# Kernel optimization log

Hardware: AMD Instinct MI355X
Metric: run time of the kernel (lower is better)

## Reference

```python
import jax, jax.numpy as jnp
import numpy as np

NUM_HEADS = 16

def _apply_rope(x, cos, sin):
    # x: (B, H, T, D); cos/sin: (T, D//2)
    B, H, T, D = x.shape
    xr = x.reshape(B, H, T, D // 2, 2)
    x0, x1 = xr[..., 0], xr[..., 1]
    c = cos[None, None, :, :]
    s = sin[None, None, :, :]
    out = jnp.stack([x0 * c - x1 * s, x0 * s + x1 * c], axis=-1)
    return out.reshape(B, H, T, D)


def setup_inputs() -> dict:
    key = jax.random.key(0)
    k1, k2, k3 = jax.random.split(key, 3)
    B, T, C = 2, 2048, 1024
    D = C // NUM_HEADS
    x = jax.random.normal(k1, (B, T, C), dtype=jnp.float32)
    qkv_w = jax.random.normal(k2, (3 * C, C), dtype=jnp.float32) * (C ** -0.5)
    proj_w = jax.random.normal(k3, (C, C), dtype=jnp.float32) * (C ** -0.5)
    # standard RoPE frequency table (theta = 10000)
    inv_freq = 1.0 / (10000.0 ** (jnp.arange(0, D, 2, dtype=jnp.float32) / D))  # (D/2,)
    angles = jnp.arange(T, dtype=jnp.float32)[:, None] * inv_freq[None, :]      # (T, D/2)
    return {
        "x": x,
        "freqs_cos": jnp.cos(angles),
        "freqs_sin": jnp.sin(angles),
        "qkv_w": qkv_w,
        "proj_w": proj_w,
    }


def reference(x, freqs_cos, freqs_sin, qkv_w, proj_w):
    B, T, C = x.shape
    H = NUM_HEADS
    D = C // H
    qkv = x @ qkv_w.T                                  # (B, T, 3C)
    q, k, v = jnp.split(qkv, 3, axis=-1)
    q = q.reshape(B, T, H, D).transpose(0, 2, 1, 3)    # (B, H, T, D)
    k = k.reshape(B, T, H, D).transpose(0, 2, 1, 3)
    v = v.reshape(B, T, H, D).transpose(0, 2, 1, 3)
    q = _apply_rope(q, freqs_cos, freqs_sin)
    k = _apply_rope(k, freqs_cos, freqs_sin)
    scale = 1.0 / jnp.sqrt(jnp.asarray(D, dtype=x.dtype))
    scores = jnp.einsum('bhqd,bhkd->bhqk', q, k) * scale
    causal = jnp.tril(jnp.ones((T, T), dtype=bool))
    scores = jnp.where(causal[None, None], scores, jnp.finfo(scores.dtype).min)
    attn = jax.nn.softmax(scores, axis=-1)
    out = jnp.einsum('bhqk,bhkd->bhqd', attn, v)       # (B, H, T, D)
    out = out.transpose(0, 2, 1, 3).reshape(B, T, C)
    return out @ proj_w.T
```

## Files before the change

kernel.cpp:

```cpp
#include <hip/hip_runtime.h>
#include <stdint.h>

#define DI __device__ __forceinline__

typedef unsigned short u16;
typedef __bf16 bf16x8 __attribute__((ext_vector_type(8)));
typedef unsigned short u16x8 __attribute__((ext_vector_type(8)));
typedef unsigned short u16x4 __attribute__((ext_vector_type(4)));
typedef float f32x4 __attribute__((ext_vector_type(4)));

DI u16 f2bf(float f) { __bf16 h = (__bf16)f; return __builtin_bit_cast(u16, h); }
DI float bf2f(u16 u) { return (float)__builtin_bit_cast(__bf16, u); }

DI bf16x8 ld8(const u16* p) { return __builtin_bit_cast(bf16x8, *(const u16x8*)p); }

DI f32x4 mfma16(bf16x8 a, bf16x8 b, f32x4 c) {
  return __builtin_amdgcn_mfma_f32_16x16x32_bf16(a, b, c, 0, 0, 0);
}

DI void async16(const u16* g, u16* l) {
  __builtin_amdgcn_global_load_lds((const __attribute__((address_space(1))) void*)g,
                                   (__attribute__((address_space(3))) void*)l, 16, 0, 0);
}

__global__ __launch_bounds__(256) void cast_all(const float* __restrict__ x,
                                                const float* __restrict__ qw,
                                                const float* __restrict__ pw,
                                                u16* __restrict__ xb, u16* __restrict__ qwb,
                                                u16* __restrict__ pwb) {
  const int bi = blockIdx.x;
  const float* src;
  u16* dst;
  int off;
  if (bi < 4096) {
    src = x; dst = xb; off = bi;
  } else if (bi < 7168) {
    src = qw; dst = qwb; off = bi - 4096;
  } else {
    src = pw; dst = pwb; off = bi - 7168;
  }
  const int i = off * 256 + threadIdx.x;
  const float4 v = ((const float4*)src)[i];
  u16x4 o = {f2bf(v.x), f2bf(v.y), f2bf(v.z), f2bf(v.w)};
  ((u16x4*)dst)[i] = o;
}

template <int OUT_BF16>
__global__ __launch_bounds__(256) void gemm_bt(const u16* __restrict__ A,
                                               const u16* __restrict__ W,
                                               void* __restrict__ outp,
                                               int M, int N, int K) {
  __shared__ u16 sA[2 * 4096];
  __shared__ u16 sB[2 * 4096];
  const int tid = threadIdx.x;
  const int w = tid >> 6, L = tid & 63;
  const int lo = L & 15, quad = L >> 4;
  const int nb = N >> 7;
  const int bm = blockIdx.x / nb, bn = blockIdx.x - bm * nb;
  const int m0 = bm << 7, n0 = bn << 7;
  const int wm = (w >> 1) << 6, wn = (w & 1) << 6;

  f32x4 acc[4][4];
#pragma unroll
  for (int i = 0; i < 4; ++i)
#pragma unroll
    for (int j = 0; j < 4; ++j) acc[i][j] = 0.f;

  const int r0 = tid >> 2, s0 = tid & 3;
  const int c0 = s0 ^ ((r0 >> 1) & 3);
  const int r1 = r0 + 64;
  const int c1 = s0 ^ ((r1 >> 1) & 3);
  const u16* aP0 = A + (size_t)(m0 + r0) * K + c0 * 8;
  const u16* aP1 = A + (size_t)(m0 + r1) * K + c1 * 8;
  const u16* bP0 = W + (size_t)(n0 + r0) * K + c0 * 8;
  const u16* bP1 = W + (size_t)(n0 + r1) * K + c1 * 8;
  u16* ldA0 = &sA[tid * 8];
  u16* ldA1 = &sA[(tid + 256) * 8];
  u16* ldB0 = &sB[tid * 8];
  u16* ldB1 = &sB[(tid + 256) * 8];

  int raf[4], rbf[4];
#pragma unroll
  for (int mt = 0; mt < 4; ++mt) {
    int r = wm + mt * 16 + lo;
    raf[mt] = r * 32 + ((quad ^ ((r >> 1) & 3)) << 3);
    r = wn + mt * 16 + lo;
    rbf[mt] = r * 32 + ((quad ^ ((r >> 1) & 3)) << 3);
  }

  auto stage = [&](int buf) {
    const int bo = buf << 12;
    async16(aP0, ldA0 + bo);
    async16(aP1, ldA1 + bo);
    async16(bP0, ldB0 + bo);
    async16(bP1, ldB1 + bo);
    aP0 += 32; aP1 += 32; bP0 += 32; bP1 += 32;
  };

  const int kIters = K >> 5;
  stage(0);
  for (int kt = 0; kt < kIters; ++kt) {
    __syncthreads();
    if (kt + 1 < kIters) stage((kt + 1) & 1);
    const int bo = (kt & 1) << 12;
    bf16x8 af[4], bfr[4];
#pragma unroll
    for (int mt = 0; mt < 4; ++mt) af[mt] = ld8(&sA[bo + raf[mt]]);
#pragma unroll
    for (int nt = 0; nt < 4; ++nt) bfr[nt] = ld8(&sB[bo + rbf[nt]]);
#pragma unroll
    for (int mt = 0; mt < 4; ++mt)
#pragma unroll
      for (int nt = 0; nt < 4; ++nt)
        acc[mt][nt] = mfma16(af[mt], bfr[nt], acc[mt][nt]);
  }

#pragma unroll
  for (int mt = 0; mt < 4; ++mt) {
    const int m = m0 + wm + mt * 16 + quad * 4;
#pragma unroll
    for (int nt = 0; nt < 4; ++nt) {
      const int n = n0 + wn + nt * 16 + lo;
#pragma unroll
      for (int r = 0; r < 4; ++r) {
        const size_t off = (size_t)(m + r) * N + n;
        if (OUT_BF16)
          ((u16*)outp)[off] = f2bf(acc[mt][nt][r]);
        else
          ((float*)outp)[off] = acc[mt][nt][r];
      }
    }
  }
}

#define QSCALE 0.18033688011112f
__global__ __launch_bounds__(256) void ropevt_k(const u16* __restrict__ qkv,
                                                const float* __restrict__ cosb,
                                                const float* __restrict__ sinb,
                                                u16* __restrict__ qo, u16* __restrict__ ko,
                                                u16* __restrict__ vto) {
  __shared__ u16 sT[64 * 64];
  const int tid = threadIdx.x;
  if (blockIdx.x < 8192) {
    const int idx = blockIdx.x * 256 + tid;
    const int i = idx & 31;
    const int t = (idx >> 5) & 2047;
    const int h = (idx >> 16) & 15;
    const int b = idx >> 20;
    const size_t src = ((size_t)(b * 2048 + t)) * 3072 + h * 64 + 2 * i;
    const float q0v = bf2f(qkv[src]), q1v = bf2f(qkv[src + 1]);
    const float k0v = bf2f(qkv[src + 1024]), k1v = bf2f(qkv[src + 1025]);
    const float c = cosb[t * 32 + i], s = sinb[t * 32 + i];
    const size_t dst = ((size_t)((b * 16 + h) * 2048 + t)) * 64 + 2 * i;
    qo[dst] = f2bf((q0v * c - q1v * s) * QSCALE);
    qo[dst + 1] = f2bf((q0v * s + q1v * c) * QSCALE);
    ko[dst] = f2bf(k0v * c - k1v * s);
    ko[dst + 1] = f2bf(k0v * s + k1v * c);
  } else {
    const int bi = blockIdx.x - 8192;
    const int bh = bi & 31;
    const int t0 = (bi >> 5) << 6;
    const int b = bh >> 4, h = bh & 15;
#pragma unroll
    for (int it = 0; it < 2; ++it) {
      const int id = tid + it * 256;
      const int tr = id >> 3, s = id & 7, c = s ^ (tr & 7);
      async16(qkv + (size_t)(b * 2048 + t0 + tr) * 3072 + 2048 + h * 64 + c * 8, &sT[id * 8]);
    }
    __syncthreads();
#pragma unroll
    for (int it = 0; it < 2; ++it) {
      const int id = tid + it * 256;
      const int d = id >> 3, ct = id & 7;
      u16x8 o;
#pragma unroll
      for (int j = 0; j < 8; ++j) {
        const int t = ct * 8 + j;
        o[j] = sT[t * 64 + (((d >> 3) ^ (t & 7)) << 3) + (d & 7)];
      }
      *(u16x8*)(vto + ((size_t)bh * 64 + d) * 2048 + t0 + ct * 8) = o;
    }
  }
}

__global__ __launch_bounds__(256) void fattn_part(const u16* __restrict__ qs,
                                                  const u16* __restrict__ ks,
                                                  const u16* __restrict__ vtb,
                                                  u16* __restrict__ opart,
                                                  float* __restrict__ lbuf) {
  __shared__ u16 sK[2 * 4096];
  __shared__ u16 sVt[2 * 4096];
  __shared__ u16 sP[4][16 * 64];
  const int tid = threadIdx.x;
  const int w = tid >> 6, L = tid & 63;
  const int lo = L & 15, quad = L >> 4;
  const int raw = blockIdx.x;
  const int part = raw & 1;
  const int bh = (raw >> 1) & 31;
  const int qi = 31 - (raw >> 6);
  const int n = qi + 1;
  const int h0 = (n + 1) >> 1;
  const int tk0 = part ? h0 : 0;
  const int tk1 = part ? n : h0;
  const size_t hoff = (size_t)bh * (2048 * 64);
  const int wq = (qi << 6) + w * 16;
  u16* sPw = sP[w];

  const int kvA = tid >> 3, cA = (tid & 7) ^ (kvA & 7);
  const int idB = tid + 256;
  const int kvB = idB >> 3, cB = (idB & 7) ^ (kvB & 7);
  const u16* kP0 = ks + hoff + (size_t)(tk0 * 64 + kvA) * 64 + cA * 8;
  const u16* kP1 = ks + hoff + (size_t)(tk0 * 64 + kvB) * 64 + cB * 8;
  const u16* vP0 = vtb + hoff + (size_t)kvA * 2048 + tk0 * 64 + cA * 8;
  const u16* vP1 = vtb + hoff + (size_t)kvB * 2048 + tk0 * 64 + cB * 8;
  u16* ldK0 = &sK[tid * 8];
  u16* ldK1 = &sK[idB * 8];
  u16* ldV0 = &sVt[tid * 8];
  u16* ldV1 = &sVt[idB * 8];

  auto stage = [&](int buf) {
    const int bo = buf << 12;
    async16(kP0, ldK0 + bo);
    async16(kP1, ldK1 + bo);
    async16(vP0, ldV0 + bo);
    async16(vP1, ldV1 + bo);
    kP0 += 4096; kP1 += 4096; vP0 += 64; vP1 += 64;
  };

  int kaOff[4][2], pOff[2], pwOff[4];
#pragma unroll
  for (int mt = 0; mt < 4; ++mt) {
    const int kv = mt * 16 + lo;
#pragma unroll
    for (int kd = 0; kd < 2; ++kd) {
      const int c = kd * 4 + quad;
      kaOff[mt][kd] = kv * 64 + ((c ^ (kv & 7)) << 3);
    }
    const int c2 = 2 * mt + (quad >> 1);
    pwOff[mt] = lo * 64 + ((c2 ^ (lo & 7)) << 3) + (quad & 1) * 4;
  }
#pragma unroll
  for (int kh = 0; kh < 2; ++kh) pOff[kh] = lo * 64 + (((kh * 4 + quad) ^ (lo & 7)) << 3);

  bf16x8 qb[2];
#pragma unroll
  for (int kd = 0; kd < 2; ++kd)
    qb[kd] = ld8(qs + hoff + (size_t)(wq + lo) * 64 + kd * 32 + quad * 8);

  bf16x8 ones;
#pragma unroll
  for (int j = 0; j < 8; ++j) ones[j] = (__bf16)1.0f;

  f32x4 lacc = 0.f;
  f32x4 ot[4];
#pragma unroll
  for (int mt = 0; mt < 4; ++mt) ot[mt] = 0.f;

  const int ntk = tk1 - tk0;
  if (ntk > 0) stage(0);
  for (int it2 = 0; it2 < ntk; ++it2) {
    __syncthreads();
    if (it2 + 1 < ntk) stage((it2 + 1) & 1);
    const int bo = (it2 & 1) << 12;
    const int kt = tk0 + it2;

    f32x4 st[4];
#pragma unroll
    for (int mt = 0; mt < 4; ++mt) st[mt] = 0.f;
#pragma unroll
    for (int mt = 0; mt < 4; ++mt)
#pragma unroll
      for (int kd = 0; kd < 2; ++kd)
        st[mt] = mfma16(ld8(&sK[bo + kaOff[mt][kd]]), qb[kd], st[mt]);

    if (kt == qi) {
      const int qg = wq + lo;
      const int kv0 = kt << 6;
#pragma unroll
      for (int mt = 0; mt < 4; ++mt)
#pragma unroll
        for (int r = 0; r < 4; ++r) {
          const int kvg = kv0 + mt * 16 + quad * 4 + r;
          if (kvg > qg) st[mt][r] = -3.0e38f;
        }
    }
#pragma unroll
    for (int mt = 0; mt < 4; ++mt) {
      u16x4 pk = {f2bf(__builtin_amdgcn_exp2f(st[mt][0])),
                  f2bf(__builtin_amdgcn_exp2f(st[mt][1])),
                  f2bf(__builtin_amdgcn_exp2f(st[mt][2])),
                  f2bf(__builtin_amdgcn_exp2f(st[mt][3]))};
      *(u16x4*)&sPw[pwOff[mt]] = pk;
    }
    asm volatile("s_waitcnt lgkmcnt(0)" ::: "memory");
    bf16x8 pbf[2];
#pragma unroll
    for (int kh = 0; kh < 2; ++kh) pbf[kh] = ld8(&sPw[pOff[kh]]);
    lacc = mfma16(ones, pbf[0], lacc);
    lacc = mfma16(ones, pbf[1], lacc);
#pragma unroll
    for (int mt = 0; mt < 4; ++mt)
#pragma unroll
      for (int kh = 0; kh < 2; ++kh)
        ot[mt] = mfma16(ld8(&sVt[bo + kaOff[mt][kh]]), pbf[kh], ot[mt]);
  }

  const int pq = bh * 32 + qi;
  u16* obase = opart + (size_t)(part * 1024 + pq) * 4096 + (size_t)(w * 16 + lo) * 64;
#pragma unroll
  for (int mt = 0; mt < 4; ++mt) {
    const int d0 = mt * 16 + quad * 4;
    u16x4 ok = {f2bf(ot[mt][0]), f2bf(ot[mt][1]), f2bf(ot[mt][2]), f2bf(ot[mt][3])};
    *(u16x4*)&obase[d0] = ok;
  }
  if (quad == 0) lbuf[(size_t)(part * 1024 + pq) * 64 + w * 16 + lo] = lacc[0];
}

__global__ __launch_bounds__(256) void fattn_merge(const u16* __restrict__ opart,
                                                   const float* __restrict__ lbuf,
                                                   u16* __restrict__ aout) {
  const int pq = blockIdx.x;
  const int bh = pq >> 5, qi = pq & 31;
  const int b = bh >> 4, h = bh & 15;
  const int tid = threadIdx.x;
#pragma unroll
  for (int it = 0; it < 2; ++it) {
    const int idx = tid + it * 256;
    const int q = idx >> 3, d0 = (idx & 7) * 8;
    const float l0 = lbuf[(size_t)pq * 64 + q];
    const float l1 = lbuf[(size_t)(1024 + pq) * 64 + q];
    const float inv = 1.f / (l0 + l1);
    const u16x8 o0 = *(const u16x8*)&opart[(size_t)pq * 4096 + q * 64 + d0];
    const u16x8 o1 = *(const u16x8*)&opart[(size_t)(1024 + pq) * 4096 + q * 64 + d0];
    u16x8 o;
#pragma unroll
    for (int j = 0; j < 8; ++j) o[j] = f2bf((bf2f(o0[j]) + bf2f(o1[j])) * inv);
    *(u16x8*)&aout[((size_t)(b * 2048 + qi * 64 + q)) * 1024 + h * 64 + d0] = o;
  }
}

extern "C" void kernel_launch(void* const* d_in, const int* in_sizes, int n_in,
                              void* d_out, int out_size, void* d_ws, size_t ws_size,
                              hipStream_t stream) {
  const float* x = (const float*)d_in[0];
  const float* fcos = (const float*)d_in[1];
  const float* fsin = (const float*)d_in[2];
  const float* qkvw = (const float*)d_in[3];
  const float* projw = (const float*)d_in[4];
  float* out = (float*)d_out;

  char* ws = (char*)d_ws;
  u16* x_bf = (u16*)(ws);
  u16* qkvw_bf = (u16*)(ws + (8u << 20));
  u16* projw_bf = (u16*)(ws + (14u << 20));
  u16* qkv_bf = (u16*)(ws + (16u << 20));
  u16* q_bf = (u16*)(ws + (40u << 20));
  u16* k_bf = (u16*)(ws + (48u << 20));
  u16* vt = (u16*)(ws + (56u << 20));
  u16* attn_bf = (u16*)(ws + (64u << 20));
  u16* opart = (u16*)(ws + (16u << 20));
  float* lbuf = (float*)(ws + (32u << 20));

  cast_all<<<8192, 256, 0, stream>>>(x, qkvw, projw, x_bf, qkvw_bf, projw_bf);
  gemm_bt<1><<<768, 256, 0, stream>>>(x_bf, qkvw_bf, (void*)qkv_bf, 4096, 3072, 1024);
  ropevt_k<<<9216, 256, 0, stream>>>(qkv_bf, fcos, fsin, q_bf, k_bf, vt);
  fattn_part<<<2048, 256, 0, stream>>>(q_bf, k_bf, vt, opart, lbuf);
  fattn_merge<<<1024, 256, 0, stream>>>(opart, lbuf, attn_bf);
  gemm_bt<0><<<256, 256, 0, stream>>>(attn_bf, projw_bf, (void*)out, 4096, 1024, 1024);
}
```

Before: 189.8 us.

## Rewrite flash attention with 32x32 MFMA, 128-row query blocks, register P transpose

```diff
diff --git a/kernel.cpp b/kernel.cpp
--- a/kernel.cpp
+++ b/kernel.cpp
@@ -8,6 +8,9 @@
 typedef unsigned short u16x8 __attribute__((ext_vector_type(8)));
 typedef unsigned short u16x4 __attribute__((ext_vector_type(4)));
 typedef float f32x4 __attribute__((ext_vector_type(4)));
+typedef float f32x16 __attribute__((ext_vector_type(16)));
+typedef unsigned int u32x2 __attribute__((ext_vector_type(2)));
+typedef unsigned int u32x4 __attribute__((ext_vector_type(4)));
 
 DI u16 f2bf(float f) { __bf16 h = (__bf16)f; return __builtin_bit_cast(u16, h); }
 DI float bf2f(u16 u) { return (float)__builtin_bit_cast(__bf16, u); }
@@ -16,6 +19,15 @@
 
 DI f32x4 mfma16(bf16x8 a, bf16x8 b, f32x4 c) {
   return __builtin_amdgcn_mfma_f32_16x16x32_bf16(a, b, c, 0, 0, 0);
+}
+DI f32x16 mfma32(bf16x8 a, bf16x8 b, f32x16 c) {
+  return __builtin_amdgcn_mfma_f32_32x32x16_bf16(a, b, c, 0, 0, 0);
+}
+
+DI unsigned pkbf(float a, float b) {
+  unsigned r;
+  asm("v_cvt_pk_bf16_f32 %0, %1, %2" : "=v"(r) : "v"(a), "v"(b));
+  return r;
 }
 
 DI void async16(const u16* g, u16* l) {
@@ -183,28 +195,27 @@
   }
 }
 
-__global__ __launch_bounds__(256) void fattn_part(const u16* __restrict__ qs,
-                                                  const u16* __restrict__ ks,
-                                                  const u16* __restrict__ vtb,
-                                                  u16* __restrict__ opart,
-                                                  float* __restrict__ lbuf) {
+__global__ __launch_bounds__(256, 2) void fattn_part(const u16* __restrict__ qs,
+                                                     const u16* __restrict__ ks,
+                                                     const u16* __restrict__ vtb,
+                                                     u16* __restrict__ opart,
+                                                     float* __restrict__ lbuf) {
   __shared__ u16 sK[2 * 4096];
   __shared__ u16 sVt[2 * 4096];
-  __shared__ u16 sP[4][16 * 64];
   const int tid = threadIdx.x;
   const int w = tid >> 6, L = tid & 63;
-  const int lo = L & 15, quad = L >> 4;
+  const int col = L & 31, hi = L >> 5;
   const int raw = blockIdx.x;
   const int part = raw & 1;
   const int bh = (raw >> 1) & 31;
-  const int qi = 31 - (raw >> 6);
-  const int n = qi + 1;
-  const int h0 = (n + 1) >> 1;
+  const int qb = 15 - (raw >> 6);
+  const int n = 2 * qb + 2;
+  const int h0 = qb + 1;
   const int tk0 = part ? h0 : 0;
   const int tk1 = part ? n : h0;
   const size_t hoff = (size_t)bh * (2048 * 64);
-  const int wq = (qi << 6) + w * 16;
-  u16* sPw = sP[w];
+  const int q0 = qb << 7;
+  const int wq = q0 + w * 32;
 
   const int kvA = tid >> 3, cA = (tid & 7) ^ (kvA & 7);
   const int idB = tid + 256;
@@ -227,93 +238,101 @@
     kP0 += 4096; kP1 += 4096; vP0 += 64; vP1 += 64;
   };
 
-  int kaOff[4][2], pOff[2], pwOff[4];
-#pragma unroll
-  for (int mt = 0; mt < 4; ++mt) {
-    const int kv = mt * 16 + lo;
-#pragma unroll
-    for (int kd = 0; kd < 2; ++kd) {
-      const int c = kd * 4 + quad;
-      kaOff[mt][kd] = kv * 64 + ((c ^ (kv & 7)) << 3);
-    }
-    const int c2 = 2 * mt + (quad >> 1);
-    pwOff[mt] = lo * 64 + ((c2 ^ (lo & 7)) << 3) + (quad & 1) * 4;
-  }
-#pragma unroll
-  for (int kh = 0; kh < 2; ++kh) pOff[kh] = lo * 64 + (((kh * 4 + quad) ^ (lo & 7)) << 3);
-
-  bf16x8 qb[2];
-#pragma unroll
-  for (int kd = 0; kd < 2; ++kd)
-    qb[kd] = ld8(qs + hoff + (size_t)(wq + lo) * 64 + kd * 32 + quad * 8);
+  int kaOff[2][4];
+#pragma unroll
+  for (int mt = 0; mt < 2; ++mt) {
+    const int row = mt * 32 + col;
+#pragma unroll
+    for (int ksI = 0; ksI < 4; ++ksI)
+      kaOff[mt][ksI] = row * 64 + (((ksI * 2 + hi) ^ (row & 7)) << 3);
+  }
+
+  bf16x8 qf[4];
+#pragma unroll
+  for (int ksI = 0; ksI < 4; ++ksI)
+    qf[ksI] = ld8(qs + hoff + (size_t)(wq + col) * 64 + ksI * 16 + hi * 8);
 
   bf16x8 ones;
 #pragma unroll
   for (int j = 0; j < 8; ++j) ones[j] = (__bf16)1.0f;
 
-  f32x4 lacc = 0.f;
-  f32x4 ot[4];
-#pragma unroll
-  for (int mt = 0; mt < 4; ++mt) ot[mt] = 0.f;
+  f32x16 lacc = 0.f;
+  f32x16 ot0 = 0.f, ot1 = 0.f;
 
   const int ntk = tk1 - tk0;
-  if (ntk > 0) stage(0);
+  stage(0);
   for (int it2 = 0; it2 < ntk; ++it2) {
     __syncthreads();
     if (it2 + 1 < ntk) stage((it2 + 1) & 1);
     const int bo = (it2 & 1) << 12;
     const int kt = tk0 + it2;
 
-    f32x4 st[4];
-#pragma unroll
-    for (int mt = 0; mt < 4; ++mt) st[mt] = 0.f;
-#pragma unroll
-    for (int mt = 0; mt < 4; ++mt)
-#pragma unroll
-      for (int kd = 0; kd < 2; ++kd)
-        st[mt] = mfma16(ld8(&sK[bo + kaOff[mt][kd]]), qb[kd], st[mt]);
-
-    if (kt == qi) {
-      const int qg = wq + lo;
-      const int kv0 = kt << 6;
-#pragma unroll
-      for (int mt = 0; mt < 4; ++mt)
-#pragma unroll
-        for (int r = 0; r < 4; ++r) {
-          const int kvg = kv0 + mt * 16 + quad * 4 + r;
-          if (kvg > qg) st[mt][r] = -3.0e38f;
+    if (64 * kt <= wq + 31) {
+      f32x16 st0 = 0.f, st1 = 0.f;
+#pragma unroll
+      for (int ksI = 0; ksI < 4; ++ksI) {
+        st0 = mfma32(ld8(&sK[bo + kaOff[0][ksI]]), qf[ksI], st0);
+        st1 = mfma32(ld8(&sK[bo + kaOff[1][ksI]]), qf[ksI], st1);
+      }
+      if (64 * kt + 63 > wq) {
+        const int qg = wq + col;
+        const int kvb = 64 * kt + 4 * hi;
+#pragma unroll
+        for (int r = 0; r < 16; ++r) {
+          const int kvr = kvb + (r & 3) + 8 * (r >> 2);
+          if (kvr > qg) st0[r] = -3.0e38f;
+          if (kvr + 32 > qg) st1[r] = -3.0e38f;
         }
-    }
-#pragma unroll
-    for (int mt = 0; mt < 4; ++mt) {
-      u16x4 pk = {f2bf(__builtin_amdgcn_exp2f(st[mt][0])),
-                  f2bf(__builtin_amdgcn_exp2f(st[mt][1])),
-                  f2bf(__builtin_amdgcn_exp2f(st[mt][2])),
-                  f2bf(__builtin_amdgcn_exp2f(st[mt][3]))};
-      *(u16x4*)&sPw[pwOff[mt]] = pk;
-    }
-    asm volatile("s_waitcnt lgkmcnt(0)" ::: "memory");
-    bf16x8 pbf[2];
-#pragma unroll
-    for (int kh = 0; kh < 2; ++kh) pbf[kh] = ld8(&sPw[pOff[kh]]);
-    lacc = mfma16(ones, pbf[0], lacc);
-    lacc = mfma16(ones, pbf[1], lacc);
-#pragma unroll
-    for (int mt = 0; mt < 4; ++mt)
-#pragma unroll
-      for (int kh = 0; kh < 2; ++kh)
-        ot[mt] = mfma16(ld8(&sVt[bo + kaOff[mt][kh]]), pbf[kh], ot[mt]);
-  }
-
-  const int pq = bh * 32 + qi;
-  u16* obase = opart + (size_t)(part * 1024 + pq) * 4096 + (size_t)(w * 16 + lo) * 64;
-#pragma unroll
-  for (int mt = 0; mt < 4; ++mt) {
-    const int d0 = mt * 16 + quad * 4;
-    u16x4 ok = {f2bf(ot[mt][0]), f2bf(ot[mt][1]), f2bf(ot[mt][2]), f2bf(ot[mt][3])};
-    *(u16x4*)&obase[d0] = ok;
-  }
-  if (quad == 0) lbuf[(size_t)(part * 1024 + pq) * 64 + w * 16 + lo] = lacc[0];
+      }
+      bf16x8 pf[4];
+#pragma unroll
+      for (int mt = 0; mt < 2; ++mt) {
+        const f32x16 sv = mt ? st1 : st0;
+        f32x16 p;
+#pragma unroll
+        for (int r = 0; r < 16; ++r) p[r] = __builtin_amdgcn_exp2f(sv[r]);
+        {
+          unsigned x0 = pkbf(p[0], p[1]), x1 = pkbf(p[2], p[3]);
+          unsigned y0 = pkbf(p[4], p[5]), y1 = pkbf(p[6], p[7]);
+          u32x2 r02 = __builtin_amdgcn_permlane32_swap(x0, y0, false, false);
+          u32x2 r13 = __builtin_amdgcn_permlane32_swap(x1, y1, false, false);
+          u32x4 wv = {r02[0], r13[0], r02[1], r13[1]};
+          pf[2 * mt] = __builtin_bit_cast(bf16x8, wv);
+        }
+        {
+          unsigned x0 = pkbf(p[8], p[9]), x1 = pkbf(p[10], p[11]);
+          unsigned y0 = pkbf(p[12], p[13]), y1 = pkbf(p[14], p[15]);
+          u32x2 r02 = __builtin_amdgcn_permlane32_swap(x0, y0, false, false);
+          u32x2 r13 = __builtin_amdgcn_permlane32_swap(x1, y1, false, false);
+          u32x4 wv = {r02[0], r13[0], r02[1], r13[1]};
+          pf[2 * mt + 1] = __builtin_bit_cast(bf16x8, wv);
+        }
+      }
+#pragma unroll
+      for (int ksI = 0; ksI < 4; ++ksI) lacc = mfma32(ones, pf[ksI], lacc);
+#pragma unroll
+      for (int ksI = 0; ksI < 4; ++ksI) {
+        ot0 = mfma32(ld8(&sVt[bo + kaOff[0][ksI]]), pf[ksI], ot0);
+        ot1 = mfma32(ld8(&sVt[bo + kaOff[1][ksI]]), pf[ksI], ot1);
+      }
+    }
+  }
+
+  const int q = wq + col;
+  const int pq = bh * 32 + (q >> 6);
+  u16* ob = opart + (size_t)(part * 1024 + pq) * 4096 + (size_t)(q & 63) * 64;
+#pragma unroll
+  for (int mtd = 0; mtd < 2; ++mtd) {
+    const f32x16 o = mtd ? ot1 : ot0;
+#pragma unroll
+    for (int rg = 0; rg < 4; ++rg) {
+      const int d0 = mtd * 32 + rg * 8 + hi * 4;
+      u16x4 ok = {f2bf(o[rg * 4 + 0]), f2bf(o[rg * 4 + 1]),
+                  f2bf(o[rg * 4 + 2]), f2bf(o[rg * 4 + 3])};
+      *(u16x4*)&ob[d0] = ok;
+    }
+  }
+  if (hi == 0) lbuf[(size_t)(part * 1024 + pq) * 64 + (q & 63)] = lacc[0];
 }
 
 __global__ __launch_bounds__(256) void fattn_merge(const u16* __restrict__ opart,
@@ -364,7 +383,7 @@
   cast_all<<<8192, 256, 0, stream>>>(x, qkvw, projw, x_bf, qkvw_bf, projw_bf);
   gemm_bt<1><<<768, 256, 0, stream>>>(x_bf, qkvw_bf, (void*)qkv_bf, 4096, 3072, 1024);
   ropevt_k<<<9216, 256, 0, stream>>>(qkv_bf, fcos, fsin, q_bf, k_bf, vt);
-  fattn_part<<<2048, 256, 0, stream>>>(q_bf, k_bf, vt, opart, lbuf);
+  fattn_part<<<1024, 256, 0, stream>>>(q_bf, k_bf, vt, opart, lbuf);
   fattn_merge<<<1024, 256, 0, stream>>>(opart, lbuf, attn_bf);
   gemm_bt<0><<<256, 256, 0, stream>>>(attn_bf, projw_bf, (void*)out, 4096, 1024, 1024);
 }
```

New measurement: 186.3 us. Within noise of the previous version (-1.9%).
